# Optimization experiments

Hardware: AMD Instinct MI355X
Metric: run time of the kernel (lower is better)

The kernel has to match this reference:

```python
import jax, jax.numpy as jnp
import numpy as np

EMB = 256  # embedding_dim


def setup_inputs() -> dict:
    key = jax.random.key(0)
    k1, k2, k3 = jax.random.split(key, 3)
    B, P, N, D = 32, 4, 1024, EMB
    x = jax.random.normal(k1, (B, P, N, D), dtype=jnp.float32)
    W_qkv = jax.random.normal(k2, (D, 1 + 2 * D), dtype=jnp.float32) * (1.0 / np.sqrt(D))
    b_qkv = jnp.zeros((1 + 2 * D,), dtype=jnp.float32)
    W_o = jax.random.normal(k3, (D, D), dtype=jnp.float32) * (1.0 / np.sqrt(D))
    b_o = jnp.zeros((D,), dtype=jnp.float32)
    return {"x": x, "W_qkv": W_qkv, "b_qkv": b_qkv, "W_o": W_o, "b_o": b_o}


def reference(x, W_qkv, b_qkv, W_o, b_o):
    # x: [B, P, N, D]
    D = W_o.shape[0]
    qkv = jnp.einsum('bpnd,de->bpne', x, W_qkv) + b_qkv  # [B,P,N,1+2D]
    q = qkv[..., :1]                 # [B,P,N,1]
    k = qkv[..., 1:1 + D]            # [B,P,N,D]
    v = jax.nn.relu(qkv[..., 1 + D:])  # [B,P,N,D]
    # softmax over the patch axis N (axis=2)
    context_scores = jax.nn.softmax(q, axis=2)  # [B,P,N,1]
    # dropout layers operate in inference mode here (identity)
    context_vector = jnp.sum(k * context_scores, axis=2, keepdims=True)  # [B,P,1,D]
    updated_values = v * context_vector  # broadcast multiply, [B,P,N,D]
    final = jnp.einsum('bpnd,de->bpne', updated_values, W_o) + b_o  # [B,P,N,D]
    return final
```

## Files before the change

kernel.cpp:

```cpp
#include <hip/hip_runtime.h>


typedef float  floatx4 __attribute__((ext_vector_type(4)));
typedef __bf16 bf16x8  __attribute__((ext_vector_type(8)));
typedef unsigned short u16;
typedef u16 u16x8 __attribute__((ext_vector_type(8)));

#define NGRP 128

__device__ __forceinline__ float bf2f(u16 u) {
    union { unsigned int i; float f; } c; c.i = ((unsigned int)u) << 16; return c.f;
}
__device__ __forceinline__ u16 f2bf(float f) {
    union { __bf16 h; u16 u; } c; c.h = (__bf16)f; return c.u;
}
__device__ __forceinline__ floatx4 mfma16(bf16x8 a, bf16x8 b, floatx4 c) {
    return __builtin_amdgcn_mfma_f32_16x16x32_bf16(a, b, c, 0, 0, 0);
}

__device__ __forceinline__ void dma16(const u16* src, u16* lds) {
    __builtin_amdgcn_global_load_lds(
        (const __attribute__((address_space(1))) unsigned int*)src,
        (__attribute__((address_space(3))) unsigned int*)lds, 16, 0, 0);
}

__global__ __launch_bounds__(256) void k_prep(
    const float* __restrict__ Wqkv, const float* __restrict__ Wo,
    u16* __restrict__ Wvp, u16* __restrict__ Wop,
    float* __restrict__ wqp, float* __restrict__ y, float* __restrict__ Sg)
{
    const int i = blockIdx.x * 256 + threadIdx.x;
    const int j = i & 7, lane = (i >> 3) & 63, kk = (i >> 9) & 7, ct = i >> 12;
    const int k = kk * 32 + (lane >> 4) * 8 + j;
    Wvp[i] = f2bf(Wqkv[k * 513 + (257 + ct * 16 + (lane & 15))]);
    Wop[i] = f2bf(Wo[k * 256 + (ct * 16 + (lane & 15))]);
    if (i < 256) wqp[i] = Wqkv[i * 513];
    if (i < NGRP * 256) y[i] = 0.f;
    if (i < NGRP) Sg[i] = 0.f;
}

__global__ __launch_bounds__(256) void k_sum(
    const float* __restrict__ x, const float* __restrict__ wqp,
    const float* __restrict__ bqkv,
    float* __restrict__ y, float* __restrict__ Sg, u16* __restrict__ xb)
{
    const int tid = threadIdx.x;
    const int m0 = blockIdx.x * 64;
    const int g  = blockIdx.x >> 4;
    const int cc = tid & 31, r0 = tid >> 5;
    const int w = tid >> 6, lane = tid & 63;
    __shared__ float e_s[64];
    __shared__ float ws4[4 * 256];

    const floatx4 wq0 = *(const floatx4*)(wqp + cc * 8);
    const floatx4 wq1 = *(const floatx4*)(wqp + cc * 8 + 4);
    u16* xt = xb + (size_t)blockIdx.x * 16384;

    float qp[8];
    u16x8 o[8];
#pragma unroll
    for (int i = 0; i < 8; ++i) {
        const int row = r0 + 8 * i;
        const float* xp = x + (size_t)(m0 + row) * 256 + cc * 8;
        floatx4 u0 = *(const floatx4*)xp;
        floatx4 u1 = *(const floatx4*)(xp + 4);
        qp[i] = u0[0] * wq0[0] + u0[1] * wq0[1] + u0[2] * wq0[2] + u0[3] * wq0[3]
              + u1[0] * wq1[0] + u1[1] * wq1[1] + u1[2] * wq1[2] + u1[3] * wq1[3];
        u16x8 t;
        t[0] = f2bf(u0[0]); t[1] = f2bf(u0[1]); t[2] = f2bf(u0[2]); t[3] = f2bf(u0[3]);
        t[4] = f2bf(u1[0]); t[5] = f2bf(u1[1]); t[6] = f2bf(u1[2]); t[7] = f2bf(u1[3]);
        o[i] = t;
        *(u16x8*)(xt + row * 256 + ((cc ^ (row & 15)) * 8)) = t;
    }

#pragma unroll
    for (int m = 1; m <= 16; m <<= 1) {
#pragma unroll
        for (int i = 0; i < 8; ++i) qp[i] += __shfl_xor(qp[i], m, 64);
    }
    if ((tid & 31) == 0) {
        const float bq0 = bqkv[0];
#pragma unroll
        for (int i = 0; i < 8; ++i) e_s[r0 + 8 * i] = __expf(qp[i] + bq0);
    }
    __syncthreads();

    float yacc[8];
#pragma unroll
    for (int j = 0; j < 8; ++j) yacc[j] = 0.f;
#pragma unroll
    for (int i = 0; i < 8; ++i) {
        const float e = e_s[r0 + 8 * i];
#pragma unroll
        for (int j = 0; j < 8; ++j) yacc[j] += e * bf2f(o[i][j]);
    }
#pragma unroll
    for (int j = 0; j < 8; ++j) yacc[j] += __shfl_xor(yacc[j], 32, 64);
    if (lane < 32) {
#pragma unroll
        for (int j = 0; j < 8; ++j) ws4[w * 256 + lane * 8 + j] = yacc[j];
    }
    __syncthreads();

    if (tid < 64) {
        float e = e_s[tid];
#pragma unroll
        for (int s = 32; s > 0; s >>= 1) e += __shfl_xor(e, s, 64);
        if (tid == 0) atomicAdd(Sg + g, e);
    }
    {
        const float s = ws4[tid] + ws4[256 + tid] + ws4[512 + tid] + ws4[768 + tid];
        atomicAdd(y + g * 256 + tid, s);
    }
}

__global__ __launch_bounds__(256) void k_cv(
    const float* __restrict__ Wqkv, const float* __restrict__ bqkv,
    const float* __restrict__ y, const float* __restrict__ Sg,
    float* __restrict__ cv)
{
    const int g = blockIdx.x, d = threadIdx.x;
    __shared__ float ys[256];
    ys[d] = y[g * 256 + d] * (1.0f / Sg[g]);
    __syncthreads();
    float acc = bqkv[1 + d];
    const float* wp = Wqkv + 1 + d;
#pragma unroll 4
    for (int t = 0; t < 256; t++) acc += ys[t] * wp[(size_t)t * 513];
    cv[g * 256 + d] = acc;
}

__global__ __launch_bounds__(256, 4) void k_vo(
    const u16* __restrict__ xb, const u16* __restrict__ Wvp,
    const u16* __restrict__ Wop, const float* __restrict__ cv,
    const float* __restrict__ bqkv, const float* __restrict__ bo,
    float* __restrict__ out)
{
    const int tid = threadIdx.x;
    const int w = tid >> 6, lane = tid & 63, quad = lane >> 4, n16 = lane & 15;
    const int m = blockIdx.x;
    const int m0 = m * 32;
    const int g  = m >> 5;

    __shared__ u16 As[32 * 256];
    __shared__ float cvs[256];

    cvs[tid] = cv[g * 256 + tid];

    {
        const u16* src = xb + (size_t)m * 8192;
#pragma unroll
        for (int it = 0; it < 4; ++it)
            dma16(src + (size_t)(it * 256 + tid) * 8, &As[(it * 256 + w * 64) * 8]);
    }
    __syncthreads();

    floatx4 acc[4][2];
#pragma unroll
    for (int i = 0; i < 4; i++)
#pragma unroll
        for (int rt = 0; rt < 2; rt++) acc[i][rt] = (floatx4){0.f, 0.f, 0.f, 0.f};
#pragma unroll
    for (int kk = 0; kk < 8; kk++) {
        bf16x8 a[2];
#pragma unroll
        for (int rt = 0; rt < 2; rt++) {
            const int row = rt * 16 + n16;
            a[rt] = __builtin_bit_cast(bf16x8,
                *(const u16x8*)(&As[row * 256 + (((kk * 4 + quad) ^ n16) * 8)]));
        }
#pragma unroll
        for (int i = 0; i < 4; i++) {
            const int ct = w + 4 * i;
            bf16x8 bfr = __builtin_bit_cast(bf16x8,
                *(const u16x8*)(Wvp + (size_t)((ct * 8 + kk) * 64 + lane) * 8));
#pragma unroll
            for (int rt = 0; rt < 2; rt++) acc[i][rt] = mfma16(a[rt], bfr, acc[i][rt]);
        }
    }
    __syncthreads();

#pragma unroll
    for (int i = 0; i < 4; i++) {
        const int col = (w + 4 * i) * 16 + n16;
        const float bias = bqkv[257 + col];
        const float scale = cvs[col];
        const int cchunk = col >> 3, co = col & 7;
#pragma unroll
        for (int rt = 0; rt < 2; rt++) {
#pragma unroll
            for (int r = 0; r < 4; r++) {
                const int row = rt * 16 + quad * 4 + r;
                As[row * 256 + ((cchunk ^ (row & 15)) * 8) + co] =
                    f2bf(fmaxf(acc[i][rt][r] + bias, 0.f) * scale);
            }
        }
    }
    __syncthreads();

    floatx4 acc2[4][2];
#pragma unroll
    for (int i = 0; i < 4; i++)
#pragma unroll
        for (int rt = 0; rt < 2; rt++) acc2[i][rt] = (floatx4){0.f, 0.f, 0.f, 0.f};
#pragma unroll
    for (int kk = 0; kk < 8; kk++) {
        bf16x8 a[2];
#pragma unroll
        for (int rt = 0; rt < 2; rt++) {
            const int row = rt * 16 + n16;
            a[rt] = __builtin_bit_cast(bf16x8,
                *(const u16x8*)(&As[row * 256 + (((kk * 4 + quad) ^ n16) * 8)]));
        }
#pragma unroll
        for (int i = 0; i < 4; i++) {
            const int ct = w + 4 * i;
            bf16x8 bfr = __builtin_bit_cast(bf16x8,
                *(const u16x8*)(Wop + (size_t)((ct * 8 + kk) * 64 + lane) * 8));
#pragma unroll
            for (int rt = 0; rt < 2; rt++) acc2[i][rt] = mfma16(a[rt], bfr, acc2[i][rt]);
        }
    }

#pragma unroll
    for (int i = 0; i < 4; i++) {
        const int col = (w + 4 * i) * 16 + n16;
        const float bias = bo[col];
#pragma unroll
        for (int rt = 0; rt < 2; rt++) {
            const int rowb = m0 + rt * 16 + quad * 4;
#pragma unroll
            for (int r = 0; r < 4; r++)
                out[(size_t)(rowb + r) * 256 + col] = acc2[i][rt][r] + bias;
        }
    }
}

extern "C" void kernel_launch(void* const* d_in, const int* in_sizes, int n_in,
                              void* d_out, int out_size, void* d_ws, size_t ws_size,
                              hipStream_t stream)
{
    const float* x    = (const float*)d_in[0];
    const float* Wqkv = (const float*)d_in[1];
    const float* bqkv = (const float*)d_in[2];
    const float* Wo   = (const float*)d_in[3];
    const float* bo   = (const float*)d_in[4];
    float* out = (float*)d_out;

    char* ws = (char*)d_ws;
    u16*   Wvp = (u16*)(ws);
    u16*   Wop = (u16*)(ws + 131072);
    float* wqp = (float*)(ws + 262144);
    float* y   = (float*)(ws + 263168);
    float* Sg  = (float*)(ws + 394240);
    float* cv  = (float*)(ws + 394752);
    u16*   xb  = (u16*)(ws + 525824);

    k_prep<<<256,  256, 0, stream>>>(Wqkv, Wo, Wvp, Wop, wqp, y, Sg);
    k_sum <<<2048, 256, 0, stream>>>(x, wqp, bqkv, y, Sg, xb);
    k_cv  <<<NGRP, 256, 0, stream>>>(Wqkv, bqkv, y, Sg, cv);
    k_vo  <<<4096, 256, 0, stream>>>(xb, Wvp, Wop, cv, bqkv, bo, out);
}
```

Measured before the change: 328.0 us.

## Move V projection into reduction pass and fold context scale into Wo

The V projection GEMM with ReLU moves into the first pass, which already holds each x tile, so that pass writes bf16 V instead of bf16 x. The output kernel then runs a single GEMM, with the per-group context vector multiplied into the Wo fragments on the fly, and each block handles 64 rows instead of 32. This takes one GEMM stage and one LDS round trip out of the final kernel, so the V GEMM no longer waits on the context-vector step. The cost is a heavier first kernel with a 32KB LDS tile and 4x4 accumulators per wave, which may lower occupancy, plus an extra bf16 rounding of the scaled weights.

```diff
diff --git a/kernel.cpp b/kernel.cpp
--- a/kernel.cpp
+++ b/kernel.cpp
@@ -39,22 +39,22 @@
     if (i < NGRP) Sg[i] = 0.f;
 }
 
-__global__ __launch_bounds__(256) void k_sum(
+__global__ __launch_bounds__(256, 4) void k_sumv(
     const float* __restrict__ x, const float* __restrict__ wqp,
-    const float* __restrict__ bqkv,
-    float* __restrict__ y, float* __restrict__ Sg, u16* __restrict__ xb)
+    const u16* __restrict__ Wvp, const float* __restrict__ bqkv,
+    float* __restrict__ y, float* __restrict__ Sg, u16* __restrict__ vb)
 {
     const int tid = threadIdx.x;
     const int m0 = blockIdx.x * 64;
     const int g  = blockIdx.x >> 4;
     const int cc = tid & 31, r0 = tid >> 5;
-    const int w = tid >> 6, lane = tid & 63;
+    const int w = tid >> 6, lane = tid & 63, quad = lane >> 4, n16 = lane & 15;
+    __shared__ u16 As[64 * 256];
     __shared__ float e_s[64];
     __shared__ float ws4[4 * 256];
 
     const floatx4 wq0 = *(const floatx4*)(wqp + cc * 8);
     const floatx4 wq1 = *(const floatx4*)(wqp + cc * 8 + 4);
-    u16* xt = xb + (size_t)blockIdx.x * 16384;
 
     float qp[8];
     u16x8 o[8];
@@ -70,7 +70,6 @@
         t[0] = f2bf(u0[0]); t[1] = f2bf(u0[1]); t[2] = f2bf(u0[2]); t[3] = f2bf(u0[3]);
         t[4] = f2bf(u1[0]); t[5] = f2bf(u1[1]); t[6] = f2bf(u1[2]); t[7] = f2bf(u1[3]);
         o[i] = t;
-        *(u16x8*)(xt + row * 256 + ((cc ^ (row & 15)) * 8)) = t;
     }
 
 #pragma unroll
@@ -85,20 +84,27 @@
     }
     __syncthreads();
 
-    float yacc[8];
-#pragma unroll
-    for (int j = 0; j < 8; ++j) yacc[j] = 0.f;
+    {
+        float yacc[8];
+#pragma unroll
+        for (int j = 0; j < 8; ++j) yacc[j] = 0.f;
+#pragma unroll
+        for (int i = 0; i < 8; ++i) {
+            const float e = e_s[r0 + 8 * i];
+#pragma unroll
+            for (int j = 0; j < 8; ++j) yacc[j] += e * bf2f(o[i][j]);
+        }
+#pragma unroll
+        for (int j = 0; j < 8; ++j) yacc[j] += __shfl_xor(yacc[j], 32, 64);
+        if (lane < 32) {
+#pragma unroll
+            for (int j = 0; j < 8; ++j) ws4[w * 256 + lane * 8 + j] = yacc[j];
+        }
+    }
 #pragma unroll
     for (int i = 0; i < 8; ++i) {
-        const float e = e_s[r0 + 8 * i];
-#pragma unroll
-        for (int j = 0; j < 8; ++j) yacc[j] += e * bf2f(o[i][j]);
-    }
-#pragma unroll
-    for (int j = 0; j < 8; ++j) yacc[j] += __shfl_xor(yacc[j], 32, 64);
-    if (lane < 32) {
-#pragma unroll
-        for (int j = 0; j < 8; ++j) ws4[w * 256 + lane * 8 + j] = yacc[j];
+        const int row = r0 + 8 * i;
+        *(u16x8*)(As + row * 256 + ((cc ^ (row & 15)) * 8)) = o[i];
     }
     __syncthreads();
 
@@ -111,6 +117,57 @@
     {
         const float s = ws4[tid] + ws4[256 + tid] + ws4[512 + tid] + ws4[768 + tid];
         atomicAdd(y + g * 256 + tid, s);
+    }
+
+    floatx4 acc[4][4];
+#pragma unroll
+    for (int i = 0; i < 4; i++)
+#pragma unroll
+        for (int rt = 0; rt < 4; rt++) acc[i][rt] = (floatx4){0.f, 0.f, 0.f, 0.f};
+#pragma unroll
+    for (int kk = 0; kk < 8; kk++) {
+        bf16x8 a[4];
+#pragma unroll
+        for (int rt = 0; rt < 4; rt++) {
+            const int row = rt * 16 + n16;
+            a[rt] = __builtin_bit_cast(bf16x8,
+                *(const u16x8*)(&As[row * 256 + (((kk * 4 + quad) ^ n16) * 8)]));
+        }
+#pragma unroll
+        for (int i = 0; i < 4; i++) {
+            const int ct = w + 4 * i;
+            bf16x8 bfr = __builtin_bit_cast(bf16x8,
+                *(const u16x8*)(Wvp + (size_t)((ct * 8 + kk) * 64 + lane) * 8));
+#pragma unroll
+            for (int rt = 0; rt < 4; rt++) acc[i][rt] = mfma16(a[rt], bfr, acc[i][rt]);
+        }
+    }
+    __syncthreads();
+
+#pragma unroll
+    for (int i = 0; i < 4; i++) {
+        const int col = (w + 4 * i) * 16 + n16;
+        const float bias = bqkv[257 + col];
+        const int cchunk = col >> 3, co = col & 7;
+#pragma unroll
+        for (int rt = 0; rt < 4; rt++) {
+#pragma unroll
+            for (int r = 0; r < 4; r++) {
+                const int row = rt * 16 + quad * 4 + r;
+                As[row * 256 + ((cchunk ^ (row & 15)) * 8) + co] =
+                    f2bf(fmaxf(acc[i][rt][r] + bias, 0.f));
+            }
+        }
+    }
+    __syncthreads();
+
+    {
+        u16* vbt = vb + (size_t)blockIdx.x * 16384;
+#pragma unroll
+        for (int it = 0; it < 8; ++it) {
+            const int c = it * 256 + tid;
+            *(u16x8*)(vbt + c * 8) = *(const u16x8*)(As + c * 8);
+        }
     }
 }
 
@@ -130,95 +187,61 @@
     cv[g * 256 + d] = acc;
 }
 
-__global__ __launch_bounds__(256, 4) void k_vo(
-    const u16* __restrict__ xb, const u16* __restrict__ Wvp,
-    const u16* __restrict__ Wop, const float* __restrict__ cv,
-    const float* __restrict__ bqkv, const float* __restrict__ bo,
+__global__ __launch_bounds__(256, 4) void k_out(
+    const u16* __restrict__ vb, const u16* __restrict__ Wop,
+    const float* __restrict__ cv, const float* __restrict__ bo,
     float* __restrict__ out)
 {
     const int tid = threadIdx.x;
     const int w = tid >> 6, lane = tid & 63, quad = lane >> 4, n16 = lane & 15;
-    const int m = blockIdx.x;
-    const int m0 = m * 32;
-    const int g  = m >> 5;
-
-    __shared__ u16 As[32 * 256];
+    const int m0 = blockIdx.x * 64;
+    const int g  = blockIdx.x >> 4;
+
+    __shared__ u16 As[64 * 256];
     __shared__ float cvs[256];
 
     cvs[tid] = cv[g * 256 + tid];
 
     {
-        const u16* src = xb + (size_t)m * 8192;
-#pragma unroll
-        for (int it = 0; it < 4; ++it)
+        const u16* src = vb + (size_t)blockIdx.x * 16384;
+#pragma unroll
+        for (int it = 0; it < 8; ++it)
             dma16(src + (size_t)(it * 256 + tid) * 8, &As[(it * 256 + w * 64) * 8]);
     }
     __syncthreads();
 
-    floatx4 acc[4][2];
+    floatx4 acc[4][4];
 #pragma unroll
     for (int i = 0; i < 4; i++)
 #pragma unroll
-        for (int rt = 0; rt < 2; rt++) acc[i][rt] = (floatx4){0.f, 0.f, 0.f, 0.f};
+        for (int rt = 0; rt < 4; rt++) acc[i][rt] = (floatx4){0.f, 0.f, 0.f, 0.f};
+
 #pragma unroll
     for (int kk = 0; kk < 8; kk++) {
-        bf16x8 a[2];
-#pragma unroll
-        for (int rt = 0; rt < 2; rt++) {
+        bf16x8 a[4];
+#pragma unroll
+        for (int rt = 0; rt < 4; rt++) {
             const int row = rt * 16 + n16;
             a[rt] = __builtin_bit_cast(bf16x8,
                 *(const u16x8*)(&As[row * 256 + (((kk * 4 + quad) ^ n16) * 8)]));
         }
+        const floatx4 c0 = *(const floatx4*)(cvs + kk * 32 + quad * 8);
+        const floatx4 c1 = *(const floatx4*)(cvs + kk * 32 + quad * 8 + 4);
 #pragma unroll
         for (int i = 0; i < 4; i++) {
             const int ct = w + 4 * i;
-            bf16x8 bfr = __builtin_bit_cast(bf16x8,
-                *(const u16x8*)(Wvp + (size_t)((ct * 8 + kk) * 64 + lane) * 8));
-#pragma unroll
-            for (int rt = 0; rt < 2; rt++) acc[i][rt] = mfma16(a[rt], bfr, acc[i][rt]);
-        }
-    }
-    __syncthreads();
-
-#pragma unroll
-    for (int i = 0; i < 4; i++) {
-        const int col = (w + 4 * i) * 16 + n16;
-        const float bias = bqkv[257 + col];
-        const float scale = cvs[col];
-        const int cchunk = col >> 3, co = col & 7;
-#pragma unroll
-        for (int rt = 0; rt < 2; rt++) {
-#pragma unroll
-            for (int r = 0; r < 4; r++) {
-                const int row = rt * 16 + quad * 4 + r;
-                As[row * 256 + ((cchunk ^ (row & 15)) * 8) + co] =
-                    f2bf(fmaxf(acc[i][rt][r] + bias, 0.f) * scale);
-            }
-        }
-    }
-    __syncthreads();
-
-    floatx4 acc2[4][2];
-#pragma unroll
-    for (int i = 0; i < 4; i++)
-#pragma unroll
-        for (int rt = 0; rt < 2; rt++) acc2[i][rt] = (floatx4){0.f, 0.f, 0.f, 0.f};
-#pragma unroll
-    for (int kk = 0; kk < 8; kk++) {
-        bf16x8 a[2];
-#pragma unroll
-        for (int rt = 0; rt < 2; rt++) {
-            const int row = rt * 16 + n16;
-            a[rt] = __builtin_bit_cast(bf16x8,
-                *(const u16x8*)(&As[row * 256 + (((kk * 4 + quad) ^ n16) * 8)]));
-        }
-#pragma unroll
-        for (int i = 0; i < 4; i++) {
-            const int ct = w + 4 * i;
-            bf16x8 bfr = __builtin_bit_cast(bf16x8,
-                *(const u16x8*)(Wop + (size_t)((ct * 8 + kk) * 64 + lane) * 8));
-#pragma unroll
-            for (int rt = 0; rt < 2; rt++) acc2[i][rt] = mfma16(a[rt], bfr, acc2[i][rt]);
+            u16x8 wo = *(const u16x8*)(Wop + (size_t)((ct * 8 + kk) * 64 + lane) * 8);
+            bf16x8 b;
+            b[0] = (__bf16)(c0[0] * bf2f(wo[0]));
+            b[1] = (__bf16)(c0[1] * bf2f(wo[1]));
+            b[2] = (__bf16)(c0[2] * bf2f(wo[2]));
+            b[3] = (__bf16)(c0[3] * bf2f(wo[3]));
+            b[4] = (__bf16)(c1[0] * bf2f(wo[4]));
+            b[5] = (__bf16)(c1[1] * bf2f(wo[5]));
+            b[6] = (__bf16)(c1[2] * bf2f(wo[6]));
+            b[7] = (__bf16)(c1[3] * bf2f(wo[7]));
+#pragma unroll
+            for (int rt = 0; rt < 4; rt++) acc[i][rt] = mfma16(a[rt], b, acc[i][rt]);
         }
     }
 
@@ -227,11 +250,11 @@
         const int col = (w + 4 * i) * 16 + n16;
         const float bias = bo[col];
 #pragma unroll
-        for (int rt = 0; rt < 2; rt++) {
+        for (int rt = 0; rt < 4; rt++) {
             const int rowb = m0 + rt * 16 + quad * 4;
 #pragma unroll
             for (int r = 0; r < 4; r++)
-                out[(size_t)(rowb + r) * 256 + col] = acc2[i][rt][r] + bias;
+                out[(size_t)(rowb + r) * 256 + col] = acc[i][rt][r] + bias;
         }
     }
 }
@@ -254,10 +277,10 @@
     float* y   = (float*)(ws + 263168);
     float* Sg  = (float*)(ws + 394240);
     float* cv  = (float*)(ws + 394752);
-    u16*   xb  = (u16*)(ws + 525824);
+    u16*   vb  = (u16*)(ws + 525824);
 
     k_prep<<<256,  256, 0, stream>>>(Wqkv, Wo, Wvp, Wop, wqp, y, Sg);
-    k_sum <<<2048, 256, 0, stream>>>(x, wqp, bqkv, y, Sg, xb);
+    k_sumv<<<2048, 256, 0, stream>>>(x, wqp, Wvp, bqkv, y, Sg, vb);
     k_cv  <<<NGRP, 256, 0, stream>>>(Wqkv, bqkv, y, Sg, cv);
-    k_vo  <<<4096, 256, 0, stream>>>(xb, Wvp, Wop, cv, bqkv, bo, out);
-}
+    k_out <<<2048, 256, 0, stream>>>(vb, Wop, cv, bo, out);
+}
```

After: 328.4 us. Within noise of the previous version (+0.1%).

## Drop bf16 x staging buffer; convert x inside k_vo and fold prep into k_sum

Applied to the files above, without the earlier changes.

Removes the intermediate bf16 copy of x: k_vo now reads fp32 x directly and converts it into LDS, and k_sum no longer writes xb. Weight packing moves into the first blocks of k_sum and the accumulator zeroing becomes a memset, removing one kernel launch. k_vo tiles grow from 32 to 64 rows, which reuses weight fragments more but doubles LDS and accumulator registers, possibly lowering occupancy.

```diff
diff --git a/kernel.cpp b/kernel.cpp
--- a/kernel.cpp
+++ b/kernel.cpp
@@ -18,31 +18,11 @@
     return __builtin_amdgcn_mfma_f32_16x16x32_bf16(a, b, c, 0, 0, 0);
 }
 
-__device__ __forceinline__ void dma16(const u16* src, u16* lds) {
-    __builtin_amdgcn_global_load_lds(
-        (const __attribute__((address_space(1))) unsigned int*)src,
-        (__attribute__((address_space(3))) unsigned int*)lds, 16, 0, 0);
-}
-
-__global__ __launch_bounds__(256) void k_prep(
-    const float* __restrict__ Wqkv, const float* __restrict__ Wo,
-    u16* __restrict__ Wvp, u16* __restrict__ Wop,
-    float* __restrict__ wqp, float* __restrict__ y, float* __restrict__ Sg)
-{
-    const int i = blockIdx.x * 256 + threadIdx.x;
-    const int j = i & 7, lane = (i >> 3) & 63, kk = (i >> 9) & 7, ct = i >> 12;
-    const int k = kk * 32 + (lane >> 4) * 8 + j;
-    Wvp[i] = f2bf(Wqkv[k * 513 + (257 + ct * 16 + (lane & 15))]);
-    Wop[i] = f2bf(Wo[k * 256 + (ct * 16 + (lane & 15))]);
-    if (i < 256) wqp[i] = Wqkv[i * 513];
-    if (i < NGRP * 256) y[i] = 0.f;
-    if (i < NGRP) Sg[i] = 0.f;
-}
-
-__global__ __launch_bounds__(256) void k_sum(
-    const float* __restrict__ x, const float* __restrict__ wqp,
-    const float* __restrict__ bqkv,
-    float* __restrict__ y, float* __restrict__ Sg, u16* __restrict__ xb)
+__global__ __launch_bounds__(256, 4) void k_sum(
+    const float* __restrict__ x, const float* __restrict__ Wqkv,
+    const float* __restrict__ Wo, const float* __restrict__ bqkv,
+    float* __restrict__ y, float* __restrict__ Sg,
+    u16* __restrict__ Wvp, u16* __restrict__ Wop)
 {
     const int tid = threadIdx.x;
     const int m0 = blockIdx.x * 64;
@@ -52,9 +32,20 @@
     __shared__ float e_s[64];
     __shared__ float ws4[4 * 256];
 
-    const floatx4 wq0 = *(const floatx4*)(wqp + cc * 8);
-    const floatx4 wq1 = *(const floatx4*)(wqp + cc * 8 + 4);
-    u16* xt = xb + (size_t)blockIdx.x * 16384;
+    if (blockIdx.x < 256) {
+        const int i = blockIdx.x * 256 + tid;
+        const int j = i & 7, pl = (i >> 3) & 63, kk = (i >> 9) & 7, ct = i >> 12;
+        const int k = kk * 32 + (pl >> 4) * 8 + j;
+        Wvp[i] = f2bf(Wqkv[k * 513 + (257 + ct * 16 + (pl & 15))]);
+        Wop[i] = f2bf(Wo[k * 256 + (ct * 16 + (pl & 15))]);
+    }
+
+    float wqv[8];
+    {
+        const float* wb = Wqkv + (size_t)(cc * 8) * 513;
+#pragma unroll
+        for (int j = 0; j < 8; ++j) wqv[j] = wb[(size_t)j * 513];
+    }
 
     float qp[8];
     u16x8 o[8];
@@ -64,13 +55,12 @@
         const float* xp = x + (size_t)(m0 + row) * 256 + cc * 8;
         floatx4 u0 = *(const floatx4*)xp;
         floatx4 u1 = *(const floatx4*)(xp + 4);
-        qp[i] = u0[0] * wq0[0] + u0[1] * wq0[1] + u0[2] * wq0[2] + u0[3] * wq0[3]
-              + u1[0] * wq1[0] + u1[1] * wq1[1] + u1[2] * wq1[2] + u1[3] * wq1[3];
+        qp[i] = u0[0] * wqv[0] + u0[1] * wqv[1] + u0[2] * wqv[2] + u0[3] * wqv[3]
+              + u1[0] * wqv[4] + u1[1] * wqv[5] + u1[2] * wqv[6] + u1[3] * wqv[7];
         u16x8 t;
         t[0] = f2bf(u0[0]); t[1] = f2bf(u0[1]); t[2] = f2bf(u0[2]); t[3] = f2bf(u0[3]);
         t[4] = f2bf(u1[0]); t[5] = f2bf(u1[1]); t[6] = f2bf(u1[2]); t[7] = f2bf(u1[3]);
         o[i] = t;
-        *(u16x8*)(xt + row * 256 + ((cc ^ (row & 15)) * 8)) = t;
     }
 
 #pragma unroll
@@ -131,40 +121,45 @@
 }
 
 __global__ __launch_bounds__(256, 4) void k_vo(
-    const u16* __restrict__ xb, const u16* __restrict__ Wvp,
+    const float* __restrict__ x, const u16* __restrict__ Wvp,
     const u16* __restrict__ Wop, const float* __restrict__ cv,
     const float* __restrict__ bqkv, const float* __restrict__ bo,
     float* __restrict__ out)
 {
     const int tid = threadIdx.x;
     const int w = tid >> 6, lane = tid & 63, quad = lane >> 4, n16 = lane & 15;
-    const int m = blockIdx.x;
-    const int m0 = m * 32;
-    const int g  = m >> 5;
-
-    __shared__ u16 As[32 * 256];
+    const int m0 = blockIdx.x * 64;
+    const int g  = blockIdx.x >> 4;
+    const int cc = tid & 31, r0 = tid >> 5;
+
+    __shared__ u16 As[64 * 256];
     __shared__ float cvs[256];
 
     cvs[tid] = cv[g * 256 + tid];
 
-    {
-        const u16* src = xb + (size_t)m * 8192;
-#pragma unroll
-        for (int it = 0; it < 4; ++it)
-            dma16(src + (size_t)(it * 256 + tid) * 8, &As[(it * 256 + w * 64) * 8]);
-    }
-    __syncthreads();
-
-    floatx4 acc[4][2];
+#pragma unroll
+    for (int i = 0; i < 8; ++i) {
+        const int row = r0 + 8 * i;
+        const float* xp = x + (size_t)(m0 + row) * 256 + cc * 8;
+        floatx4 u0 = *(const floatx4*)xp;
+        floatx4 u1 = *(const floatx4*)(xp + 4);
+        u16x8 t;
+        t[0] = f2bf(u0[0]); t[1] = f2bf(u0[1]); t[2] = f2bf(u0[2]); t[3] = f2bf(u0[3]);
+        t[4] = f2bf(u1[0]); t[5] = f2bf(u1[1]); t[6] = f2bf(u1[2]); t[7] = f2bf(u1[3]);
+        *(u16x8*)(As + row * 256 + ((cc ^ (row & 15)) * 8)) = t;
+    }
+    __syncthreads();
+
+    floatx4 acc[4][4];
 #pragma unroll
     for (int i = 0; i < 4; i++)
 #pragma unroll
-        for (int rt = 0; rt < 2; rt++) acc[i][rt] = (floatx4){0.f, 0.f, 0.f, 0.f};
+        for (int rt = 0; rt < 4; rt++) acc[i][rt] = (floatx4){0.f, 0.f, 0.f, 0.f};
 #pragma unroll
     for (int kk = 0; kk < 8; kk++) {
-        bf16x8 a[2];
-#pragma unroll
-        for (int rt = 0; rt < 2; rt++) {
+        bf16x8 a[4];
+#pragma unroll
+        for (int rt = 0; rt < 4; rt++) {
             const int row = rt * 16 + n16;
             a[rt] = __builtin_bit_cast(bf16x8,
                 *(const u16x8*)(&As[row * 256 + (((kk * 4 + quad) ^ n16) * 8)]));
@@ -175,7 +170,7 @@
             bf16x8 bfr = __builtin_bit_cast(bf16x8,
                 *(const u16x8*)(Wvp + (size_t)((ct * 8 + kk) * 64 + lane) * 8));
 #pragma unroll
-            for (int rt = 0; rt < 2; rt++) acc[i][rt] = mfma16(a[rt], bfr, acc[i][rt]);
+            for (int rt = 0; rt < 4; rt++) acc[i][rt] = mfma16(a[rt], bfr, acc[i][rt]);
         }
     }
     __syncthreads();
@@ -187,7 +182,7 @@
         const float scale = cvs[col];
         const int cchunk = col >> 3, co = col & 7;
 #pragma unroll
-        for (int rt = 0; rt < 2; rt++) {
+        for (int rt = 0; rt < 4; rt++) {
 #pragma unroll
             for (int r = 0; r < 4; r++) {
                 const int row = rt * 16 + quad * 4 + r;
@@ -198,16 +193,16 @@
     }
     __syncthreads();
 
-    floatx4 acc2[4][2];
+    floatx4 acc2[4][4];
 #pragma unroll
     for (int i = 0; i < 4; i++)
 #pragma unroll
-        for (int rt = 0; rt < 2; rt++) acc2[i][rt] = (floatx4){0.f, 0.f, 0.f, 0.f};
+        for (int rt = 0; rt < 4; rt++) acc2[i][rt] = (floatx4){0.f, 0.f, 0.f, 0.f};
 #pragma unroll
     for (int kk = 0; kk < 8; kk++) {
-        bf16x8 a[2];
-#pragma unroll
-        for (int rt = 0; rt < 2; rt++) {
+        bf16x8 a[4];
+#pragma unroll
+        for (int rt = 0; rt < 4; rt++) {
             const int row = rt * 16 + n16;
             a[rt] = __builtin_bit_cast(bf16x8,
                 *(const u16x8*)(&As[row * 256 + (((kk * 4 + quad) ^ n16) * 8)]));
@@ -218,7 +213,7 @@
             bf16x8 bfr = __builtin_bit_cast(bf16x8,
                 *(const u16x8*)(Wop + (size_t)((ct * 8 + kk) * 64 + lane) * 8));
 #pragma unroll
-            for (int rt = 0; rt < 2; rt++) acc2[i][rt] = mfma16(a[rt], bfr, acc2[i][rt]);
+            for (int rt = 0; rt < 4; rt++) acc2[i][rt] = mfma16(a[rt], bfr, acc2[i][rt]);
         }
     }
 
@@ -227,7 +222,7 @@
         const int col = (w + 4 * i) * 16 + n16;
         const float bias = bo[col];
 #pragma unroll
-        for (int rt = 0; rt < 2; rt++) {
+        for (int rt = 0; rt < 4; rt++) {
             const int rowb = m0 + rt * 16 + quad * 4;
 #pragma unroll
             for (int r = 0; r < 4; r++)
@@ -250,14 +245,12 @@
     char* ws = (char*)d_ws;
     u16*   Wvp = (u16*)(ws);
     u16*   Wop = (u16*)(ws + 131072);
-    float* wqp = (float*)(ws + 262144);
-    float* y   = (float*)(ws + 263168);
-    float* Sg  = (float*)(ws + 394240);
-    float* cv  = (float*)(ws + 394752);
-    u16*   xb  = (u16*)(ws + 525824);
-
-    k_prep<<<256,  256, 0, stream>>>(Wqkv, Wo, Wvp, Wop, wqp, y, Sg);
-    k_sum <<<2048, 256, 0, stream>>>(x, wqp, bqkv, y, Sg, xb);
-    k_cv  <<<NGRP, 256, 0, stream>>>(Wqkv, bqkv, y, Sg, cv);
-    k_vo  <<<4096, 256, 0, stream>>>(xb, Wvp, Wop, cv, bqkv, bo, out);
-}
+    float* cv  = (float*)(ws + 262144);
+    float* y   = (float*)(ws + 393216);
+    float* Sg  = (float*)(ws + 524288);
+
+    hipMemsetAsync(ws + 393216, 0, 131584, stream);
+    k_sum<<<2048, 256, 0, stream>>>(x, Wqkv, Wo, bqkv, y, Sg, Wvp, Wop);
+    k_cv <<<NGRP, 256, 0, stream>>>(Wqkv, bqkv, y, Sg, cv);
+    k_vo <<<2048, 256, 0, stream>>>(x, Wvp, Wop, cv, bqkv, bo, out);
+}
```

After: 339.7 us. 3.6% more time.
